# Performance work log

Hardware: AMD Instinct MI355X
Metric: run time of the kernel (lower is better)

The kernel has to match this reference:

```python
import jax, jax.numpy as jnp
import numpy as np

L = 4        # num_layers
H = 1024     # hidden_size
NH = 16      # num_heads
KVH = 4      # num_kv_heads
QPK = NH // KVH
HD = H // NH # head_dim = 64
FF = 4096    # intermediate_size
V = 32000    # vocab_size
B, S = 2, 2048
EPS = 1e-5
STD = 0.02


def layernorm(x, g, b):
    m = jnp.mean(x, axis=-1, keepdims=True)
    v = jnp.mean(jnp.square(x - m), axis=-1, keepdims=True)
    return (x - m) * jax.lax.rsqrt(v + EPS) * g + b


def setup_inputs() -> dict:
    key = jax.random.key(0)
    ks = iter(jax.random.split(key, 24))
    n = lambda shape: STD * jax.random.normal(next(ks), shape, dtype=jnp.float32)
    KV = H * KVH // NH  # kv_size = 256
    inp = {
        'input_ids': jax.random.randint(next(ks), (B, S), 0, V),
        'attention_mask': jnp.zeros((B, S), dtype=jnp.float32),
        'tok_emb': n((V, H)),
        'pos_emb': n((S, H)),
        # per-layer stacked weights, stored [in, out] so y = x @ W + b
        'Wq': n((L, H, H)),  'bq': jnp.zeros((L, H)),
        'Wk': n((L, H, KV)), 'bk': jnp.zeros((L, KV)),
        'Wv': n((L, H, KV)), 'bv': jnp.zeros((L, KV)),
        'Wo': n((L, H, H)),  'bo': jnp.zeros((L, H)),
        'W1': n((L, H, FF)), 'b1': jnp.zeros((L, FF)),
        'W2': n((L, FF, H)), 'b2': jnp.zeros((L, H)),
        'ln1_g': jnp.ones((L, H)), 'ln1_b': jnp.zeros((L, H)),
        'ln2_g': jnp.ones((L, H)), 'ln2_b': jnp.zeros((L, H)),
        'lnf_g': jnp.ones((H,)),   'lnf_b': jnp.zeros((H,)),
        'Whead': n((H, V)),  # head has no bias
    }
    return inp


def gpt_forward(input_ids, attention_mask, tok_emb, pos_emb,
                Wq, bq, Wk, bk, Wv, bv, Wo, bo,
                W1, b1, W2, b2, ln1_g, ln1_b, ln2_g, ln2_b,
                lnf_g, lnf_b, Whead):
    b, s = input_ids.shape
    x = tok_emb[input_ids] + pos_emb[None, :s, :]  # [b,s,H]
    mask = attention_mask[:, None, None, None, :]  # [b,1,1,1,s] additive
    scale = 1.0 / jnp.sqrt(jnp.float32(HD))
    for l in range(L):
        h = layernorm(x, ln1_g[l], ln1_b[l])
        q = h @ Wq[l] + bq[l]                              # [b,s,H]
        k = h @ Wk[l] + bk[l]                              # [b,s,KV]
        v = h @ Wv[l] + bv[l]
        q = q.reshape(b, s, KVH, QPK, HD).transpose(0, 2, 3, 1, 4)  # [b,g,q,s,d]
        k = k.reshape(b, s, KVH, HD).transpose(0, 2, 1, 3)          # [b,g,s,d]
        v = v.reshape(b, s, KVH, HD).transpose(0, 2, 1, 3)
        scores = jnp.einsum('bgqsd,bgkd->bgqsk', q, k) * scale      # [b,g,q,s,s]
        scores = scores + mask
        w = jax.nn.softmax(scores, axis=-1)
        o = jnp.einsum('bgqsk,bgkd->bgqsd', w, v)                   # [b,g,q,s,d]
        o = o.transpose(0, 3, 1, 2, 4).reshape(b, s, H)
        x = x + (o @ Wo[l] + bo[l])
        h2 = layernorm(x, ln2_g[l], ln2_b[l])
        ff = jax.nn.gelu(h2 @ W1[l] + b1[l], approximate=False) @ W2[l] + b2[l]
        x = x + ff
    x = layernorm(x, lnf_g, lnf_b)
    return x @ Whead  # [b,s,V] logits


def reference(input_ids, attention_mask, tok_emb, pos_emb,
              Wq, bq, Wk, bk, Wv, bv, Wo, bo,
              W1, b1, W2, b2, ln1_g, ln1_b, ln2_g, ln2_b,
              lnf_g, lnf_b, Whead):
    return gpt_forward(input_ids, attention_mask, tok_emb, pos_emb,
                       Wq, bq, Wk, bk, Wv, bv, Wo, bo,
                       W1, b1, W2, b2, ln1_g, ln1_b, ln2_g, ln2_b,
                       lnf_g, lnf_b, Whead)
```

## Files before the change

kernel.cpp:

```cpp
#include <hip/hip_runtime.h>
#include <hip/hip_bf16.h>

#define LAYERS 4
#define H 1024
#define NH 16
#define KVH 4
#define HD 64
#define KVD 256
#define FF 4096
#define VOC 32000
#define BB 2
#define SS 2048
#define MROWS (BB*SS)
#define QKVN 1536

typedef __attribute__((ext_vector_type(4))) float f32x4;
typedef __attribute__((ext_vector_type(8))) short short8;
typedef __attribute__((ext_vector_type(4))) unsigned short u16x4;
typedef __attribute__((ext_vector_type(2))) unsigned int u32x2;

__device__ inline unsigned short f2bf(float f){
  union { float f; unsigned u; } v; v.f = f;
  return (unsigned short)((v.u + 0x7FFFu + ((v.u >> 16) & 1u)) >> 16);
}
__device__ inline unsigned cvt_pk_bf16(float a, float b){
  unsigned r;
  asm("v_cvt_pk_bf16_f32 %0, %1, %2" : "=v"(r) : "v"(a), "v"(b));
  return r;
}

__global__ __launch_bounds__(256) void embed_kernel(const int* __restrict__ ids,
    const float* __restrict__ tok, const float* __restrict__ pos, float* __restrict__ x)
{
  int row = blockIdx.x;
  int s = row & (SS-1);
  int id = ids[row];
  int t = threadIdx.x;
  f32x4 a = *(const f32x4*)&tok[(size_t)id*H + t*4];
  f32x4 p = *(const f32x4*)&pos[(size_t)s*H + t*4];
  *(f32x4*)&x[(size_t)row*H + t*4] = a + p;
}

__global__ __launch_bounds__(256) void ln_kernel(const float* __restrict__ x,
    const float* __restrict__ g, const float* __restrict__ b, unsigned short* __restrict__ out)
{
  int row = blockIdx.x;
  int t = threadIdx.x;
  const float* xr = x + (size_t)row*H;
  f32x4 v = *(const f32x4*)&xr[t*4];
  float s  = v[0]+v[1]+v[2]+v[3];
  float s2 = v[0]*v[0]+v[1]*v[1]+v[2]*v[2]+v[3]*v[3];
  #pragma unroll
  for (int off=1; off<64; off<<=1){ s += __shfl_xor(s,off); s2 += __shfl_xor(s2,off); }
  __shared__ float red[8];
  int w = t>>6;
  if ((t&63)==0){ red[w]=s; red[4+w]=s2; }
  __syncthreads();
  float S1 = red[0]+red[1]+red[2]+red[3];
  float S2 = red[4]+red[5]+red[6]+red[7];
  float mean = S1 * (1.0f/H);
  float var  = S2 * (1.0f/H) - mean*mean;
  float rs = rsqrtf(var + 1e-5f);
  u16x4 o;
  #pragma unroll
  for (int i=0;i<4;i++) o[i] = f2bf((v[i]-mean)*rs*g[t*4+i] + b[t*4+i]);
  *(u16x4*)&out[(size_t)row*H + t*4] = o;
}

__global__ __launch_bounds__(256) void convT_kernel(const float* __restrict__ in,
    unsigned short* __restrict__ out, int K, int N, size_t istride, size_t ostride)
{
  __shared__ float t[32][33];
  in  += (size_t)blockIdx.z * istride;
  out += (size_t)blockIdx.z * ostride;
  int n0 = blockIdx.x*32, k0 = blockIdx.y*32;
  int x = threadIdx.x & 31, y = threadIdx.x >> 5;
  #pragma unroll
  for (int j=0;j<4;j++) t[y+j*8][x] = in[(size_t)(k0+y+j*8)*N + n0 + x];
  __syncthreads();
  int x2 = threadIdx.x & 15, y2 = threadIdx.x >> 4;
  #pragma unroll
  for (int j=0;j<2;j++){
    int n = y2 + j*16;
    unsigned lo = f2bf(t[x2*2][n]);
    unsigned hi = f2bf(t[x2*2+1][n]);
    *(unsigned*)&out[(size_t)(n0+n)*K + k0 + x2*2] = lo | (hi<<16);
  }
}

__global__ __launch_bounds__(256) void bcat_kernel(const float* __restrict__ bq,
    const float* __restrict__ bk, const float* __restrict__ bv, float* __restrict__ out)
{
  int l = blockIdx.x, t = threadIdx.x;
  #pragma unroll
  for (int i=0;i<4;i++) out[l*QKVN + t + i*256] = bq[l*H + t + i*256];
  out[l*QKVN + 1024 + t] = bk[l*KVD + t];
  out[l*QKVN + 1280 + t] = bv[l*KVD + t];
}

template<int EPI>
__global__ __launch_bounds__(512, 4) void gemm_bt(
    const unsigned short* __restrict__ A, const unsigned short* __restrict__ Bt,
    const float* __restrict__ bias, const float* __restrict__ res,
    float* __restrict__ outf, unsigned short* __restrict__ outb,
    unsigned short* __restrict__ outb2, unsigned short* __restrict__ outb3, int N, int K)
{
  __shared__ __align__(16) char lds[65536];
  const int tid = threadIdx.x;
  const int lane = tid & 63, wid = tid >> 6;
  const int wr = (wid>>2)*64, wc = (wid&3)*32;
  const int fr = lane & 15, fq = lane >> 4;
  const int m0 = blockIdx.x*128, n0 = blockIdx.y*128;
  const int nt = K >> 5;
  f32x4 acc[4][2] = {};

  #define STG1(PTR, baserow, kt, ldsoff) do {                                   \
    int rr = tid>>2;                                                            \
    int ss = (tid&3) ^ ((rr>>1)&3);                                             \
    __builtin_amdgcn_global_load_lds(                                           \
      (const __attribute__((address_space(1))) void*)((PTR) + (size_t)((baserow)+rr)*K + (kt)*32 + ss*8), \
      (__attribute__((address_space(3))) void*)(lds + (ldsoff) + wid*1024), 16, 0, 0); \
  } while(0)
  #define RDA1(buf,row) (*(const short8*)(lds + (buf)*16384 + (row)*64 + ((fq ^ (((row)>>1)&3))*16)))
  #define RDB1(buf,row) (*(const short8*)(lds + (buf)*16384 + 8192 + (row)*64 + ((fq ^ (((row)>>1)&3))*16)))

  STG1(A,  m0, 0, 0);      STG1(Bt, n0, 0, 8192);
  STG1(A,  m0, 1, 16384);  STG1(Bt, n0, 1, 16384+8192);
  STG1(A,  m0, 2, 32768);  STG1(Bt, n0, 2, 32768+8192);
  asm volatile("s_waitcnt vmcnt(4)" ::: "memory");
  __builtin_amdgcn_s_barrier();

  short8 a[4], b[2];
  #pragma unroll
  for (int mi=0;mi<4;mi++) a[mi] = RDA1(0, wr+mi*16+fr);
  b[0] = RDB1(0, wc+fr);
  b[1] = RDB1(0, wc+16+fr);

  for (int t = 0; t < nt; ++t){
    const int s3 = (t+3) & 3;
    const int nb = (t+1) & 3;
    const int t3 = (t+3 < nt) ? t+3 : nt-1;
    STG1(A,  m0, t3, s3*16384);
    STG1(Bt, n0, t3, s3*16384+8192);
    __builtin_amdgcn_s_setprio(1);
    #pragma unroll
    for (int mi=0;mi<4;mi++)
      acc[mi][0] = __builtin_amdgcn_mfma_f32_16x16x32_bf16(a[mi], b[0], acc[mi][0], 0,0,0);
    __builtin_amdgcn_s_setprio(0);
    asm volatile("s_waitcnt lgkmcnt(0)" ::: "memory");
    asm volatile("s_waitcnt vmcnt(4)" ::: "memory");
    __builtin_amdgcn_s_barrier();
    short8 na[4], nb0, nb1;
    nb0 = RDB1(nb, wc+fr);
    nb1 = RDB1(nb, wc+16+fr);
    #pragma unroll
    for (int mi=0;mi<4;mi++) na[mi] = RDA1(nb, wr+mi*16+fr);
    __builtin_amdgcn_s_setprio(1);
    #pragma unroll
    for (int mi=0;mi<4;mi++)
      acc[mi][1] = __builtin_amdgcn_mfma_f32_16x16x32_bf16(a[mi], b[1], acc[mi][1], 0,0,0);
    __builtin_amdgcn_s_setprio(0);
    b[0] = nb0; b[1] = nb1;
    #pragma unroll
    for (int mi=0;mi<4;mi++) a[mi] = na[mi];
  }
  #undef STG1
  #undef RDA1
  #undef RDB1

  #pragma unroll
  for (int mi=0;mi<4;mi++)
    #pragma unroll
    for (int ni=0;ni<2;ni++){
      int col = n0 + wc + ni*16 + fr;
      float bi = (EPI==3) ? 0.0f : bias[col];
      #pragma unroll
      for (int r=0;r<4;r++){
        int row = m0 + wr + mi*16 + fq*4 + r;
        float vv = acc[mi][ni][r] + bi;
        if (EPI==1)      { size_t idx=(size_t)row*N+col; outf[idx] = vv + res[idx]; }
        else if (EPI==2) { size_t idx=(size_t)row*N+col; outb[idx] = f2bf(0.5f*vv*(1.0f+erff(vv*0.70710678118f))); }
        else if (EPI==3) { size_t idx=(size_t)row*N+col; outf[idx] = vv; }
        else if (EPI==5) {
          if (col < 1024)      outb [(size_t)row*H + col]            = f2bf(vv);
          else if (col < 1280) outb2[(size_t)row*KVD + (col-1024)]   = f2bf(vv);
          else                 outb3[(size_t)(col-1280)*MROWS + row] = f2bf(vv);
        }
      }
    }
}

template<int EPI>
__global__ __launch_bounds__(512, 2) void gemm256(
    const unsigned short* __restrict__ A, const unsigned short* __restrict__ Bt,
    const float* __restrict__ bias, float* __restrict__ outf,
    unsigned short* __restrict__ outb, int N, int K)
{
  __shared__ __align__(16) char lds[131072];
  const int tid = threadIdx.x;
  const int lane = tid & 63, wid = tid >> 6;
  const int wrr = wid >> 2, wc = wid & 3;
  const int fr = lane & 15, fq = lane >> 4;
  const int m0 = blockIdx.x*256, n0 = blockIdx.y*256;
  const int nt = K >> 5;
  f32x4 acc[8][4] = {};

  #define STG(PTR, baserow, kt, ldsoff) do {                                    \
    _Pragma("unroll")                                                           \
    for (int c=0;c<2;c++){                                                      \
      int rr = c*128 + (tid>>2);                                                \
      int ss = (tid&3) ^ ((rr>>1)&3);                                           \
      __builtin_amdgcn_global_load_lds(                                         \
        (const __attribute__((address_space(1))) void*)((PTR) + (size_t)((baserow)+rr)*K + (kt)*32 + ss*8), \
        (__attribute__((address_space(3))) void*)(lds + (ldsoff) + c*8192 + wid*1024), 16, 0, 0); \
    }                                                                           \
  } while(0)
  #define RDA(buf,row) (*(const short8*)(lds + (buf)*32768 + (row)*64 + ((fq ^ (((row)>>1)&3))*16)))
  #define RDB(buf,row) (*(const short8*)(lds + (buf)*32768 + 16384 + (row)*64 + ((fq ^ (((row)>>1)&3))*16)))

  STG(A,  m0, 0, 0);      STG(Bt, n0, 0, 16384);
  STG(A,  m0, 1, 32768);  STG(Bt, n0, 1, 32768+16384);
  STG(A,  m0, 2, 65536);  STG(Bt, n0, 2, 65536+16384);
  asm volatile("s_waitcnt vmcnt(8)" ::: "memory");
  __builtin_amdgcn_s_barrier();

  short8 a[4], b2[2];
  short8 bA = RDB(0, wc*64+fr);
  short8 bB = RDB(0, wc*64+16+fr);
  #pragma unroll
  for (int mi=0;mi<4;mi++) a[mi] = RDA(0, wrr*128+mi*16+fr);

  for (int t = 0; t < nt; ++t){
    const int buf = t & 3;
    const int s3 = (t+3) & 3;
    const int nb = (t+1) & 3;
    const int t3 = (t+3 < nt) ? t+3 : nt-1;
    short8 ah[4];
    #pragma unroll
    for (int mi=0;mi<4;mi++) ah[mi] = RDA(buf, wrr*128+(4+mi)*16+fr);
    b2[0] = RDB(buf, wc*64+32+fr);
    b2[1] = RDB(buf, wc*64+48+fr);
    STG(A, m0, t3, s3*32768);
    __builtin_amdgcn_s_setprio(1);
    #pragma unroll
    for (int mi=0;mi<4;mi++){
      acc[mi][0] = __builtin_amdgcn_mfma_f32_16x16x32_bf16(a[mi], bA, acc[mi][0], 0,0,0);
      acc[mi][1] = __builtin_amdgcn_mfma_f32_16x16x32_bf16(a[mi], bB, acc[mi][1], 0,0,0);
    }
    __builtin_amdgcn_s_setprio(0);
    STG(Bt, n0, t3, s3*32768+16384);
    __builtin_amdgcn_s_setprio(1);
    #pragma unroll
    for (int mi=0;mi<4;mi++){
      acc[4+mi][0] = __builtin_amdgcn_mfma_f32_16x16x32_bf16(ah[mi], bA, acc[4+mi][0], 0,0,0);
      acc[4+mi][1] = __builtin_amdgcn_mfma_f32_16x16x32_bf16(ah[mi], bB, acc[4+mi][1], 0,0,0);
    }
    __builtin_amdgcn_s_setprio(0);
    asm volatile("s_waitcnt lgkmcnt(0)" ::: "memory");
    asm volatile("s_waitcnt vmcnt(8)" ::: "memory");
    __builtin_amdgcn_s_barrier();
    short8 nbA = RDB(nb, wc*64+fr);
    short8 nbB = RDB(nb, wc*64+16+fr);
    short8 na[4];
    #pragma unroll
    for (int mi=0;mi<4;mi++) na[mi] = RDA(nb, wrr*128+mi*16+fr);
    __builtin_amdgcn_s_setprio(1);
    #pragma unroll
    for (int mi=0;mi<4;mi++){
      acc[mi][2] = __builtin_amdgcn_mfma_f32_16x16x32_bf16(a[mi], b2[0], acc[mi][2], 0,0,0);
      acc[mi][3] = __builtin_amdgcn_mfma_f32_16x16x32_bf16(a[mi], b2[1], acc[mi][3], 0,0,0);
    }
    __builtin_amdgcn_s_setprio(0);
    __builtin_amdgcn_s_setprio(1);
    #pragma unroll
    for (int mi=0;mi<4;mi++){
      acc[4+mi][2] = __builtin_amdgcn_mfma_f32_16x16x32_bf16(ah[mi], b2[0], acc[4+mi][2], 0,0,0);
      acc[4+mi][3] = __builtin_amdgcn_mfma_f32_16x16x32_bf16(ah[mi], b2[1], acc[4+mi][3], 0,0,0);
    }
    __builtin_amdgcn_s_setprio(0);
    bA = nbA; bB = nbB;
    #pragma unroll
    for (int mi=0;mi<4;mi++) a[mi] = na[mi];
  }
  #undef STG
  #undef RDA
  #undef RDB

  #pragma unroll
  for (int mi=0; mi<8; mi++)
    #pragma unroll
    for (int ni=0; ni<4; ni++){
      int col = n0 + wc*64 + ni*16 + fr;
      float bi = (EPI==3) ? 0.0f : bias[col];
      #pragma unroll
      for (int r=0; r<4; r++){
        int row = m0 + wrr*128 + mi*16 + fq*4 + r;
        float vv = acc[mi][ni][r] + bi;
        size_t idx = (size_t)row*N + col;
        if (EPI==3) outf[idx] = vv;
        else        outb[idx] = f2bf(0.5f*vv*(1.0f+erff(vv*0.70710678118f)));
      }
    }
}

#define LOG2E 1.4426950408889634f
__global__ __launch_bounds__(256) void attn_kernel(
    const unsigned short* __restrict__ q, const unsigned short* __restrict__ kptr,
    const unsigned short* __restrict__ vt, const float* __restrict__ mask,
    unsigned short* __restrict__ o)
{
  __shared__ char Pbuf[4][4096];
  int tid = threadIdx.x;
  int lane = tid & 63, wid = tid >> 6;
  int fr = lane & 15, fq = lane >> 4, fo = fq*8;
  int h = blockIdx.y, b = blockIdx.z, g = h >> 2;
  int qcol = h*HD, kcol = g*HD;
  int qbase = b*SS + blockIdx.x*128 + wid*32;
  char* Pl = Pbuf[wid];
  int swz = (fr & 7) << 4;

  short8 bq[2][2];
  #pragma unroll
  for (int h2=0; h2<2; h2++){
    const unsigned short* qrow = q + (size_t)(qbase + h2*16 + fr)*H + qcol;
    bq[h2][0] = *(const short8*)(qrow + fo);
    bq[h2][1] = *(const short8*)(qrow + 32 + fo);
  }

  f32x4 oacc[2][4] = {};
  float mrun[2] = {-1e30f, -1e30f}, lsum[2] = {0.f, 0.f};
  const float sc2 = 0.125f * LOG2E;

  const unsigned short* kp[4];
  #pragma unroll
  for (int f=0; f<4; f++) kp[f] = kptr + (size_t)(b*SS + f*16 + fr)*KVD + kcol + fo;
  const unsigned short* vp[4];
  #pragma unroll
  for (int dc=0; dc<4; dc++) vp[dc] = vt + (size_t)(kcol + dc*16 + fr)*MROWS + b*SS + fo;
  const float* mp = mask + b*SS + fq*4;

  short8 kaA[4][2], kaB[4][2];
  #pragma unroll
  for (int f=0; f<4; f++){
    kaA[f][0] = *(const short8*)(kp[f]);
    kaA[f][1] = *(const short8*)(kp[f] + 32);
    kp[f] += 64*KVD;
  }

#define ATTN_STEP(KA, KB, PF) do {                                             \
    f32x4 mkv[4];                                                              \
    _Pragma("unroll")                                                          \
    for (int f=0; f<4; f++) mkv[f] = *(const f32x4*)(mp + f*16);               \
    short8 va[4][2];                                                           \
    _Pragma("unroll")                                                          \
    for (int dc=0; dc<4; dc++){                                                \
      va[dc][0] = *(const short8*)(vp[dc]);                                    \
      va[dc][1] = *(const short8*)(vp[dc] + 32);                               \
    }                                                                          \
    f32x4 sf[2][4] = {};                                                       \
    __builtin_amdgcn_s_setprio(1);                                             \
    _Pragma("unroll")                                                          \
    for (int h2=0; h2<2; h2++)                                                 \
      _Pragma("unroll")                                                        \
      for (int f=0; f<4; f++){                                                 \
        sf[h2][f] = __builtin_amdgcn_mfma_f32_16x16x32_bf16(KA[f][0], bq[h2][0], sf[h2][f],0,0,0); \
        sf[h2][f] = __builtin_amdgcn_mfma_f32_16x16x32_bf16(KA[f][1], bq[h2][1], sf[h2][f],0,0,0); \
      }                                                                        \
    __builtin_amdgcn_s_setprio(0);                                             \
    if (PF){                                                                   \
      _Pragma("unroll")                                                        \
      for (int f=0; f<4; f++){                                                 \
        KB[f][0] = *(const short8*)(kp[f]);                                    \
        KB[f][1] = *(const short8*)(kp[f] + 32);                               \
        kp[f] += 64*KVD;                                                       \
      }                                                                        \
    }                                                                          \
    _Pragma("unroll")                                                          \
    for (int f=0; f<4; f++){                                                   \
      _Pragma("unroll")                                                        \
      for (int r=0; r<4; r++){                                                 \
        float m2 = mkv[f][r]*LOG2E;                                            \
        sf[0][f][r] = sf[0][f][r]*sc2 + m2;                                    \
        sf[1][f][r] = sf[1][f][r]*sc2 + m2;                                    \
      }                                                                        \
    }                                                                          \
    float pm[2];                                                               \
    _Pragma("unroll")                                                          \
    for (int h2=0; h2<2; h2++){                                                \
      float a0 = fmaxf(fmaxf(sf[h2][0][0],sf[h2][0][1]), fmaxf(sf[h2][0][2],sf[h2][0][3])); \
      float a1 = fmaxf(fmaxf(sf[h2][1][0],sf[h2][1][1]), fmaxf(sf[h2][1][2],sf[h2][1][3])); \
      float a2 = fmaxf(fmaxf(sf[h2][2][0],sf[h2][2][1]), fmaxf(sf[h2][2][2],sf[h2][2][3])); \
      float a3 = fmaxf(fmaxf(sf[h2][3][0],sf[h2][3][1]), fmaxf(sf[h2][3][2],sf[h2][3][3])); \
      float p = fmaxf(fmaxf(a0,a1), fmaxf(a2,a3));                             \
      p = fmaxf(p, __shfl_xor(p, 16));                                         \
      p = fmaxf(p, __shfl_xor(p, 32));                                         \
      pm[h2] = p;                                                              \
    }                                                                          \
    if (!__all(pm[0] <= mrun[0]+8.f && pm[1] <= mrun[1]+8.f)){                 \
      float al[2];                                                             \
      _Pragma("unroll")                                                        \
      for (int h2=0; h2<2; h2++){                                              \
        float mn = fmaxf(mrun[h2], pm[h2]);                                    \
        al[h2] = __builtin_amdgcn_exp2f(mrun[h2]-mn);                          \
        mrun[h2] = mn;                                                         \
        lsum[h2] *= al[h2];                                                    \
      }                                                                        \
      _Pragma("unroll")                                                        \
      for (int r=0; r<4; r++){                                                 \
        float altl = __shfl(al[0], fq*4+r);                                    \
        float alth = __shfl(al[1], fq*4+r);                                    \
        _Pragma("unroll")                                                      \
        for (int dc=0; dc<4; dc++){ oacc[0][dc][r]*=altl; oacc[1][dc][r]*=alth; } \
      }                                                                        \
    }                                                                          \
    _Pragma("unroll")                                                          \
    for (int h2=0; h2<2; h2++){                                                \
      float ps = 0.f;                                                          \
      _Pragma("unroll")                                                        \
      for (int f=0; f<4; f++)                                                  \
        _Pragma("unroll")                                                      \
        for (int r=0; r<4; r++){                                               \
          float e = __builtin_amdgcn_exp2f(sf[h2][f][r]-mrun[h2]);             \
          sf[h2][f][r] = e; ps += e;                                           \
        }                                                                      \
      ps += __shfl_xor(ps, 16);                                                \
      ps += __shfl_xor(ps, 32);                                                \
      lsum[h2] += ps;                                                          \
    }                                                                          \
    _Pragma("unroll")                                                          \
    for (int h2=0; h2<2; h2++){                                                \
      int prow = h2*16 + fr;                                                   \
      _Pragma("unroll")                                                        \
      for (int f=0; f<4; f++){                                                 \
        u32x2 pw;                                                              \
        pw[0] = cvt_pk_bf16(sf[h2][f][0], sf[h2][f][1]);                       \
        pw[1] = cvt_pk_bf16(sf[h2][f][2], sf[h2][f][3]);                       \
        *(u32x2*)(Pl + prow*128 + ((f*32 + fq*8) ^ swz)) = pw;                 \
      }                                                                        \
    }                                                                          \
    __builtin_amdgcn_s_setprio(1);                                             \
    _Pragma("unroll")                                                          \
    for (int h2=0; h2<2; h2++){                                                \
      int prow = h2*16 + fr;                                                   \
      _Pragma("unroll")                                                        \
      for (int gs=0; gs<2; gs++){                                              \
        short8 pa = *(const short8*)(Pl + prow*128 + ((gs*64 + fq*16) ^ swz)); \
        _Pragma("unroll")                                                      \
        for (int dc=0; dc<4; dc++)                                             \
          oacc[h2][dc] = __builtin_amdgcn_mfma_f32_16x16x32_bf16(pa, va[dc][gs], oacc[h2][dc],0,0,0); \
      }                                                                        \
    }                                                                          \
    __builtin_amdgcn_s_setprio(0);                                             \
    _Pragma("unroll")                                                          \
    for (int dc=0; dc<4; dc++) vp[dc] += 64;                                   \
    mp += 64;                                                                  \
  } while(0)

  for (int it = 0; it < SS/128 - 1; ++it){
    ATTN_STEP(kaA, kaB, 1);
    ATTN_STEP(kaB, kaA, 1);
  }
  ATTN_STEP(kaA, kaB, 1);
  ATTN_STEP(kaB, kaA, 0);
#undef ATTN_STEP

  #pragma unroll
  for (int h2=0; h2<2; h2++){
    float lt[4];
    #pragma unroll
    for (int r=0; r<4; r++) lt[r] = __shfl(lsum[h2], fq*4+r);
    #pragma unroll
    for (int dc=0; dc<4; dc++)
      #pragma unroll
      for (int r=0; r<4; r++){
        int row = qbase + h2*16 + fq*4 + r;
        o[(size_t)row*H + qcol + dc*16 + fr] = f2bf(oacc[h2][dc][r] / lt[r]);
      }
  }
}

extern "C" void kernel_launch(void* const* d_in, const int* in_sizes, int n_in,
                              void* d_out, int out_size, void* d_ws, size_t ws_size,
                              hipStream_t stream)
{
  const int*   ids  = (const int*)  d_in[0];
  const float* mask = (const float*)d_in[1];
  const float* tok  = (const float*)d_in[2];
  const float* pos  = (const float*)d_in[3];
  const float* Wq   = (const float*)d_in[4];
  const float* bq   = (const float*)d_in[5];
  const float* Wk   = (const float*)d_in[6];
  const float* bk   = (const float*)d_in[7];
  const float* Wv   = (const float*)d_in[8];
  const float* bv   = (const float*)d_in[9];
  const float* Wo   = (const float*)d_in[10];
  const float* bo   = (const float*)d_in[11];
  const float* W1   = (const float*)d_in[12];
  const float* b1   = (const float*)d_in[13];
  const float* W2   = (const float*)d_in[14];
  const float* b2   = (const float*)d_in[15];
  const float* ln1g = (const float*)d_in[16];
  const float* ln1b = (const float*)d_in[17];
  const float* ln2g = (const float*)d_in[18];
  const float* ln2b = (const float*)d_in[19];
  const float* lnfg = (const float*)d_in[20];
  const float* lnfb = (const float*)d_in[21];
  const float* Wh   = (const float*)d_in[22];
  float* out = (float*)d_out;

  char* ws = (char*)d_ws;
  float*          x    = (float*)ws;          ws += (size_t)MROWS*H*4;
  unsigned short* hb   = (unsigned short*)ws; ws += (size_t)MROWS*H*2;
  unsigned short* qb   = (unsigned short*)ws; ws += (size_t)MROWS*H*2;
  unsigned short* kb   = (unsigned short*)ws; ws += (size_t)MROWS*KVD*2;
  unsigned short* vtb  = (unsigned short*)ws; ws += (size_t)KVD*MROWS*2;
  unsigned short* ob   = (unsigned short*)ws; ws += (size_t)MROWS*H*2;
  unsigned short* f1   = (unsigned short*)ws; ws += (size_t)MROWS*FF*2;
  unsigned short* Wqkv = (unsigned short*)ws; ws += (size_t)LAYERS*QKVN*H*2;
  unsigned short* WoT  = (unsigned short*)ws; ws += (size_t)LAYERS*H*H*2;
  unsigned short* W1T  = (unsigned short*)ws; ws += (size_t)LAYERS*H*FF*2;
  unsigned short* W2T  = (unsigned short*)ws; ws += (size_t)LAYERS*H*FF*2;
  unsigned short* WhT  = (unsigned short*)ws; ws += (size_t)H*VOC*2;
  float*          bcat = (float*)ws;          ws += (size_t)LAYERS*QKVN*4;

  convT_kernel<<<dim3(H/32,   H/32,  LAYERS), 256, 0, stream>>>(Wq, Wqkv,          H,  H,   (size_t)H*H,   (size_t)QKVN*H);
  convT_kernel<<<dim3(KVD/32, H/32,  LAYERS), 256, 0, stream>>>(Wk, Wqkv + 1024*H, H,  KVD, (size_t)H*KVD, (size_t)QKVN*H);
  convT_kernel<<<dim3(KVD/32, H/32,  LAYERS), 256, 0, stream>>>(Wv, Wqkv + 1280*H, H,  KVD, (size_t)H*KVD, (size_t)QKVN*H);
  convT_kernel<<<dim3(H/32,   H/32,  LAYERS), 256, 0, stream>>>(Wo, WoT,           H,  H,   (size_t)H*H,   (size_t)H*H);
  convT_kernel<<<dim3(FF/32,  H/32,  LAYERS), 256, 0, stream>>>(W1, W1T,           H,  FF,  (size_t)H*FF,  (size_t)H*FF);
  convT_kernel<<<dim3(H/32,   FF/32, LAYERS), 256, 0, stream>>>(W2, W2T,           FF, H,   (size_t)FF*H,  (size_t)FF*H);
  convT_kernel<<<dim3(VOC/32, H/32,  1),      256, 0, stream>>>(Wh, WhT,           H,  VOC, 0, 0);
  bcat_kernel<<<LAYERS, 256, 0, stream>>>(bq, bk, bv, bcat);

  embed_kernel<<<MROWS, 256, 0, stream>>>(ids, tok, pos, x);
  for (int l=0; l<LAYERS; l++){
    ln_kernel<<<MROWS,256,0,stream>>>(x, ln1g + l*H, ln1b + l*H, hb);
    gemm_bt<5><<<dim3(MROWS/128, QKVN/128),512,0,stream>>>(hb, Wqkv + (size_t)l*QKVN*H, bcat + l*QKVN, nullptr, nullptr, qb, kb, vtb, QKVN, H);
    attn_kernel<<<dim3(SS/128, NH, BB), 256, 0, stream>>>(qb, kb, vtb, mask, ob);
    gemm_bt<1><<<dim3(MROWS/128, H/128),  512,0,stream>>>(ob, WoT + (size_t)l*H*H,  bo + l*H,  x, x, nullptr, nullptr, nullptr, H, H);
    ln_kernel<<<MROWS,256,0,stream>>>(x, ln2g + l*H, ln2b + l*H, hb);
    gemm256<2><<<dim3(MROWS/256, FF/256), 512,0,stream>>>(hb, W1T + (size_t)l*H*FF, b1 + l*FF, nullptr, f1, FF, H);
    gemm_bt<1><<<dim3(MROWS/128, H/128),  512,0,stream>>>(f1, W2T + (size_t)l*H*FF, b2 + l*H,  x, x, nullptr, nullptr, nullptr, H, FF);
  }
  ln_kernel<<<MROWS,256,0,stream>>>(x, lnfg, lnfb, hb);
  gemm256<3><<<dim3(MROWS/256, VOC/256), 512,0,stream>>>(hb, WhT, nullptr, out, nullptr, VOC, H);
}
```

Measured before the change: 1.675 ms.

## Restructure 256x256 GEMM main loop to 64-wide K tiles with double buffering

Restructures the main loop of the gemm256 kernel to step K by 64 per iteration instead of 32, using two 64KB LDS buffers instead of four 32KB stages, with an 8-way XOR swizzle over 128-byte rows. Global-to-LDS staging is split into four quarter-tile loads interleaved between four MFMA phases, with barriers between phases, in the style of an HipKittens-like 8-wave ping-pong schedule. The aim is to halve loop and barrier overhead per unit of K and to overlap loads more evenly with compute. In exchange it adds more barriers per iteration and a shallower prefetch depth, and it relies on the quarter-buffer reuse ordering being correct.

```diff
diff --git a/kernel.cpp b/kernel.cpp
--- a/kernel.cpp
+++ b/kernel.cpp
@@ -202,87 +202,101 @@
   const int wrr = wid >> 2, wc = wid & 3;
   const int fr = lane & 15, fq = lane >> 4;
   const int m0 = blockIdx.x*256, n0 = blockIdx.y*256;
-  const int nt = K >> 5;
+  const int nt = K >> 6;
   f32x4 acc[8][4] = {};
 
-  #define STG(PTR, baserow, kt, ldsoff) do {                                    \
-    _Pragma("unroll")                                                           \
-    for (int c=0;c<2;c++){                                                      \
-      int rr = c*128 + (tid>>2);                                                \
-      int ss = (tid&3) ^ ((rr>>1)&3);                                           \
-      __builtin_amdgcn_global_load_lds(                                         \
-        (const __attribute__((address_space(1))) void*)((PTR) + (size_t)((baserow)+rr)*K + (kt)*32 + ss*8), \
-        (__attribute__((address_space(3))) void*)(lds + (ldsoff) + c*8192 + wid*1024), 16, 0, 0); \
-    }                                                                           \
+  #define STGH(PTR, baserow, kt, bufb, off) do {                               \
+    _Pragma("unroll")                                                          \
+    for (int c=0;c<2;c++){                                                     \
+      int rr = c*64 + (tid>>3);                                                \
+      int sl = (tid&7) ^ (rr&7);                                               \
+      __builtin_amdgcn_global_load_lds(                                        \
+        (const __attribute__((address_space(1))) void*)((PTR) + (size_t)((baserow)+rr)*K + (size_t)(kt)*64 + sl*8), \
+        (__attribute__((address_space(3))) void*)(lds + (bufb)*65536 + (off) + c*8192 + wid*1024), 16, 0, 0); \
+    }                                                                          \
   } while(0)
-  #define RDA(buf,row) (*(const short8*)(lds + (buf)*32768 + (row)*64 + ((fq ^ (((row)>>1)&3))*16)))
-  #define RDB(buf,row) (*(const short8*)(lds + (buf)*32768 + 16384 + (row)*64 + ((fq ^ (((row)>>1)&3))*16)))
-
-  STG(A,  m0, 0, 0);      STG(Bt, n0, 0, 16384);
-  STG(A,  m0, 1, 32768);  STG(Bt, n0, 1, 32768+16384);
-  STG(A,  m0, 2, 65536);  STG(Bt, n0, 2, 65536+16384);
-  asm volatile("s_waitcnt vmcnt(8)" ::: "memory");
+  #define RDA(b, mi, ks) (*(const short8*)(lds + (b)*65536 + wrr*16384 + ((mi)*16+fr)*128 + ((((ks)*4+fq) ^ (fr&7))*16)))
+  #define RDB(b, ni, ks) (*(const short8*)(lds + (b)*65536 + 32768 + (wc>>1)*16384 + ((wc&1)*64+(ni)*16+fr)*128 + ((((ks)*4+fq) ^ (fr&7))*16)))
+
+  {
+    int t1 = (1 < nt) ? 1 : 0;
+    STGH(A,  m0,     0,  0, 0);
+    STGH(A,  m0+128, 0,  0, 16384);
+    STGH(Bt, n0,     0,  0, 32768);
+    STGH(Bt, n0+128, 0,  0, 32768+16384);
+    STGH(A,  m0,     t1, 1, 0);
+    STGH(A,  m0+128, t1, 1, 16384);
+    STGH(Bt, n0,     t1, 1, 32768);
+  }
+  asm volatile("s_waitcnt vmcnt(6)" ::: "memory");
   __builtin_amdgcn_s_barrier();
 
-  short8 a[4], b2[2];
-  short8 bA = RDB(0, wc*64+fr);
-  short8 bB = RDB(0, wc*64+16+fr);
-  #pragma unroll
-  for (int mi=0;mi<4;mi++) a[mi] = RDA(0, wrr*128+mi*16+fr);
-
   for (int t = 0; t < nt; ++t){
-    const int buf = t & 3;
-    const int s3 = (t+3) & 3;
-    const int nb = (t+1) & 3;
-    const int t3 = (t+3 < nt) ? t+3 : nt-1;
-    short8 ah[4];
-    #pragma unroll
-    for (int mi=0;mi<4;mi++) ah[mi] = RDA(buf, wrr*128+(4+mi)*16+fr);
-    b2[0] = RDB(buf, wc*64+32+fr);
-    b2[1] = RDB(buf, wc*64+48+fr);
-    STG(A, m0, t3, s3*32768);
+    const int buf = t & 1, nb = buf ^ 1;
+    const int tp1 = (t+1 < nt) ? t+1 : nt-1;
+    const int tp2 = (t+2 < nt) ? t+2 : nt-1;
+    short8 alo[4][2], ahi[4][2], blo[2][2], bhi[2][2];
+    #pragma unroll
+    for (int mi=0;mi<4;mi++){ alo[mi][0] = RDA(buf,mi,0); alo[mi][1] = RDA(buf,mi,1); }
+    #pragma unroll
+    for (int ni=0;ni<2;ni++){ blo[ni][0] = RDB(buf,ni,0); blo[ni][1] = RDB(buf,ni,1); }
+    STGH(Bt, n0+128, tp1, nb, 32768+16384);
+    __builtin_amdgcn_s_barrier();
+    asm volatile("s_waitcnt lgkmcnt(0)" ::: "memory");
     __builtin_amdgcn_s_setprio(1);
     #pragma unroll
-    for (int mi=0;mi<4;mi++){
-      acc[mi][0] = __builtin_amdgcn_mfma_f32_16x16x32_bf16(a[mi], bA, acc[mi][0], 0,0,0);
-      acc[mi][1] = __builtin_amdgcn_mfma_f32_16x16x32_bf16(a[mi], bB, acc[mi][1], 0,0,0);
-    }
+    for (int mi=0;mi<4;mi++)
+      #pragma unroll
+      for (int ni=0;ni<2;ni++){
+        acc[mi][ni] = __builtin_amdgcn_mfma_f32_16x16x32_bf16(alo[mi][0], blo[ni][0], acc[mi][ni], 0,0,0);
+        acc[mi][ni] = __builtin_amdgcn_mfma_f32_16x16x32_bf16(alo[mi][1], blo[ni][1], acc[mi][ni], 0,0,0);
+      }
     __builtin_amdgcn_s_setprio(0);
-    STG(Bt, n0, t3, s3*32768+16384);
+    __builtin_amdgcn_s_barrier();
+    #pragma unroll
+    for (int mi=0;mi<4;mi++){ ahi[mi][0] = RDA(buf,4+mi,0); ahi[mi][1] = RDA(buf,4+mi,1); }
+    __builtin_amdgcn_s_barrier();
+    asm volatile("s_waitcnt lgkmcnt(0)" ::: "memory");
     __builtin_amdgcn_s_setprio(1);
     #pragma unroll
-    for (int mi=0;mi<4;mi++){
-      acc[4+mi][0] = __builtin_amdgcn_mfma_f32_16x16x32_bf16(ah[mi], bA, acc[4+mi][0], 0,0,0);
-      acc[4+mi][1] = __builtin_amdgcn_mfma_f32_16x16x32_bf16(ah[mi], bB, acc[4+mi][1], 0,0,0);
-    }
+    for (int mi=0;mi<4;mi++)
+      #pragma unroll
+      for (int ni=0;ni<2;ni++){
+        acc[4+mi][ni] = __builtin_amdgcn_mfma_f32_16x16x32_bf16(ahi[mi][0], blo[ni][0], acc[4+mi][ni], 0,0,0);
+        acc[4+mi][ni] = __builtin_amdgcn_mfma_f32_16x16x32_bf16(ahi[mi][1], blo[ni][1], acc[4+mi][ni], 0,0,0);
+      }
     __builtin_amdgcn_s_setprio(0);
+    __builtin_amdgcn_s_barrier();
+    #pragma unroll
+    for (int ni=0;ni<2;ni++){ bhi[ni][0] = RDB(buf,2+ni,0); bhi[ni][1] = RDB(buf,2+ni,1); }
+    STGH(A, m0, tp2, buf, 0);
+    __builtin_amdgcn_s_barrier();
     asm volatile("s_waitcnt lgkmcnt(0)" ::: "memory");
-    asm volatile("s_waitcnt vmcnt(8)" ::: "memory");
-    __builtin_amdgcn_s_barrier();
-    short8 nbA = RDB(nb, wc*64+fr);
-    short8 nbB = RDB(nb, wc*64+16+fr);
-    short8 na[4];
-    #pragma unroll
-    for (int mi=0;mi<4;mi++) na[mi] = RDA(nb, wrr*128+mi*16+fr);
     __builtin_amdgcn_s_setprio(1);
     #pragma unroll
-    for (int mi=0;mi<4;mi++){
-      acc[mi][2] = __builtin_amdgcn_mfma_f32_16x16x32_bf16(a[mi], b2[0], acc[mi][2], 0,0,0);
-      acc[mi][3] = __builtin_amdgcn_mfma_f32_16x16x32_bf16(a[mi], b2[1], acc[mi][3], 0,0,0);
-    }
+    for (int mi=0;mi<4;mi++)
+      #pragma unroll
+      for (int ni=0;ni<2;ni++){
+        acc[mi][2+ni] = __builtin_amdgcn_mfma_f32_16x16x32_bf16(alo[mi][0], bhi[ni][0], acc[mi][2+ni], 0,0,0);
+        acc[mi][2+ni] = __builtin_amdgcn_mfma_f32_16x16x32_bf16(alo[mi][1], bhi[ni][1], acc[mi][2+ni], 0,0,0);
+      }
     __builtin_amdgcn_s_setprio(0);
+    __builtin_amdgcn_s_barrier();
+    STGH(A,  m0+128, tp2, buf, 16384);
+    STGH(Bt, n0,     tp2, buf, 32768);
     __builtin_amdgcn_s_setprio(1);
     #pragma unroll
-    for (int mi=0;mi<4;mi++){
-      acc[4+mi][2] = __builtin_amdgcn_mfma_f32_16x16x32_bf16(ah[mi], b2[0], acc[4+mi][2], 0,0,0);
-      acc[4+mi][3] = __builtin_amdgcn_mfma_f32_16x16x32_bf16(ah[mi], b2[1], acc[4+mi][3], 0,0,0);
-    }
+    for (int mi=0;mi<4;mi++)
+      #pragma unroll
+      for (int ni=0;ni<2;ni++){
+        acc[4+mi][2+ni] = __builtin_amdgcn_mfma_f32_16x16x32_bf16(ahi[mi][0], bhi[ni][0], acc[4+mi][2+ni], 0,0,0);
+        acc[4+mi][2+ni] = __builtin_amdgcn_mfma_f32_16x16x32_bf16(ahi[mi][1], bhi[ni][1], acc[4+mi][2+ni], 0,0,0);
+      }
     __builtin_amdgcn_s_setprio(0);
-    bA = nbA; bB = nbB;
-    #pragma unroll
-    for (int mi=0;mi<4;mi++) a[mi] = na[mi];
-  }
-  #undef STG
+    asm volatile("s_waitcnt vmcnt(6)" ::: "memory");
+    __builtin_amdgcn_s_barrier();
+  }
+  #undef STGH
   #undef RDA
   #undef RDB
 
```

Result: no change. 1.670 ms (-0.3%).
